# Kernel optimization log

Hardware: AMD Instinct MI355X
Metric: run time of the kernel (lower is better)

Reference implementation:

```python
import jax, jax.numpy as jnp
import numpy as np

B, S, D, H, V, L, N, FF = 4, 2048, 768, 4, 32000, 2048, 3, 1024
DH = D // H  # 192; note original scales scores by 1/20, not 1/sqrt(192)


def layernorm(x, g, b):
    m = jnp.mean(x, axis=-1, keepdims=True)
    v = jnp.mean((x - m) ** 2, axis=-1, keepdims=True)
    return (x - m) / jnp.sqrt(v + 1e-5) * g + b


def attn_block(h, Wq, bq, Wk, bk, Wv, bv, g, b, mask):
    Bx, Sx, _ = h.shape
    q = (h @ Wq + bq).reshape(Bx, Sx, H, DH).transpose(0, 2, 1, 3)  # bhsd
    k = (h @ Wk + bk).reshape(Bx, Sx, H, DH).transpose(0, 2, 1, 3)
    v = (h @ Wv + bv).reshape(Bx, Sx, H, DH).transpose(0, 2, 1, 3)
    w = jnp.einsum('bhqd,bhkd->bhqk', q, k) / 20.0
    w = jnp.where(mask, -1e9, w)
    # original code uses Softmax(dim=2), i.e. over the QUERY axis — kept faithful
    a = jax.nn.softmax(w, axis=2)
    o = jnp.einsum('bhqk,bhkd->bhqd', a, v)
    o = o.transpose(0, 2, 1, 3).reshape(Bx, Sx, D)
    return layernorm(h + o, g, b)


def setup_inputs() -> dict:
    key = jax.random.key(0)
    ks = jax.random.split(key, 12)
    sc = 0.02
    n = lambda k, s: jax.random.normal(k, s, jnp.float32) * sc
    return {
        'x': jax.random.randint(ks[0], (B, S), 0, V),
        'label': jax.random.randint(ks[1], (B, S), 0, V),
        'tok_emb': n(ks[2], (V, D)),
        'pos_emb': n(ks[3], (L, D)),
        'Wq': n(ks[4], (N, 2, D, D)), 'bq': jnp.zeros((N, 2, D)),
        'Wk': n(ks[5], (N, 2, D, D)), 'bk': jnp.zeros((N, 2, D)),
        'Wv': n(ks[6], (N, 2, D, D)), 'bv': jnp.zeros((N, 2, D)),
        'ln_g': jnp.ones((N, 2, D)), 'ln_b': jnp.zeros((N, 2, D)),
        'W1': n(ks[7], (N, D, FF)), 'b1': jnp.zeros((N, FF)),
        'W2': n(ks[8], (N, FF, D)), 'b2': jnp.zeros((N, D)),
        'f_g': jnp.ones((N, D)), 'f_b': jnp.zeros((N, D)),
        'Wcls': n(ks[9], (D, V)), 'bcls': jnp.zeros((V,)),
    }


def reference(x, label, tok_emb, pos_emb, Wq, bq, Wk, bk, Wv, bv, ln_g, ln_b,
              W1, b1, W2, b2, f_g, f_b, Wcls, bcls):
    Bx, Sx = x.shape
    pad = (x == 0)[:, None, :, None]                       # [B,1,S,1] masks query rows
    look = jnp.triu(jnp.ones((Sx, Sx), bool), 1)[None, None]
    mask = look | pad                                      # [B,1,S,S] -> broadcast over H
    h = tok_emb[x] + pos_emb[jnp.arange(Sx)][None, :, :]
    for i in range(N):
        for j in range(2):
            h = attn_block(h, Wq[i, j], bq[i, j], Wk[i, j], bk[i, j],
                           Wv[i, j], bv[i, j], ln_g[i, j], ln_b[i, j], mask)
        h1 = jax.nn.relu(h @ W1[i] + b1[i]) @ W2[i] + b2[i]
        h = layernorm(h + h1, f_g[i], f_b[i])
    logits = h @ Wcls + bcls                               # [B,S,V]
    logp = jax.nn.log_softmax(logits, axis=-1)
    loss = -jnp.mean(jnp.take_along_axis(logp, label[..., None], axis=-1))
    return loss
```

## Files before the change

### kernel.cpp

```cpp
#include <hip/hip_runtime.h>
#include <hip/hip_bf16.h>

using u16 = unsigned short;
using u32 = unsigned int;
using u8  = unsigned char;
using u64 = unsigned long long;
using bf16x8 = __attribute__((ext_vector_type(8))) short;
using f32x4  = __attribute__((ext_vector_type(4))) float;
using l2v    = __attribute__((ext_vector_type(2))) long;

namespace {
constexpr int BB   = 4;
constexpr int SEQ  = 2048;
constexpr int DIM  = 768;
constexpr int NH   = 4;
constexpr int DHD  = 192;
constexpr int VOC  = 32000;
constexpr int NLAY = 3;
constexpr int FFD  = 1024;
constexpr int ROWS = BB * SEQ;
constexpr int NT2  = VOC / 256;
constexpr int QKV = 3 * DIM;
constexpr int BH  = BB * NH;
}

__device__ __forceinline__ float b2f(u16 u) { return __uint_as_float(((u32)u) << 16); }
__device__ __forceinline__ u16 f2b(float f) {
    u32 x = __float_as_uint(f);
    return (u16)((x + 0x7fffu + ((x >> 16) & 1u)) >> 16);
}

__device__ __forceinline__ u32 f2e4m3(float f) {
    float af = fabsf(f);
    u32 sgn = (__float_as_uint(f) >> 24) & 0x80u;
    if (!(af < 448.f)) return sgn | 0x7Eu;
    int e = (int)((__float_as_uint(af) >> 23) & 0xff) - 127;
    if (e < -6) e = -6;
    float sc = __uint_as_float((u32)(130 - e) << 23);
    int code = __float2int_rn(af * sc) + ((e + 6) << 3);
    return sgn | (u32)code;
}

__device__ __forceinline__ void gload16(const u16* g, u16* l) {
    __builtin_amdgcn_global_load_lds(
        (const __attribute__((address_space(1))) u32*)g,
        (__attribute__((address_space(3))) u32*)l, 16, 0, 0);
}
__device__ __forceinline__ void gload16b(const u8* g, u8* l) {
    __builtin_amdgcn_global_load_lds(
        (const __attribute__((address_space(1))) u32*)g,
        (__attribute__((address_space(3))) u32*)l, 16, 0, 0);
}

#define PHASE_END(N) do {                                        \
    __builtin_amdgcn_sched_barrier(0);                           \
    asm volatile("s_waitcnt vmcnt(" #N ")" ::: "memory");        \
    __builtin_amdgcn_s_barrier();                                \
    asm volatile("" ::: "memory");                               \
    __builtin_amdgcn_sched_barrier(0);                           \
} while (0)

__device__ __forceinline__ float block_sum256(float v, float* sb) {
    #pragma unroll
    for (int off = 32; off > 0; off >>= 1) v += __shfl_down(v, off, 64);
    int lane = threadIdx.x & 63, w = threadIdx.x >> 6;
    if (lane == 0) sb[w] = v;
    __syncthreads();
    float r = sb[0] + sb[1] + sb[2] + sb[3];
    __syncthreads();
    return r;
}

template<int MODE>
__global__ __launch_bounds__(512, 2)
void gemm256(const u16* __restrict__ A, long lda,
             const u16* __restrict__ Bt, long ldb,
             int M, int N, int K,
             u16* __restrict__ Cb, long ldc,
             int HH, long sAb, long sAh, long sBb, long sBh, long sCb, long sCh,
             const int* __restrict__ xtok, float* __restrict__ cpart)
{
    __shared__ __align__(16) u16 sA[2][256 * 64];
    __shared__ __align__(16) u16 sB[2][256 * 64];

    int t = threadIdx.x, w = t >> 6, lane = t & 63;
    int wr = w >> 2, wcn = w & 3;
    int lr = lane & 15, lg = lane >> 4, rsw = lr & 7;

    int z = blockIdx.z;
    int bz = z / HH, hz = z % HH;
    const u16* Ab = A + (size_t)bz * sAb + (size_t)hz * sAh;
    const u16* Bb = Bt + (size_t)bz * sBb + (size_t)hz * sBh;
    size_t Coff = (size_t)bz * sCb + (size_t)hz * sCh;

    int bx = blockIdx.x, by = blockIdx.y;
    {
        int tix = blockIdx.x;
        by = 7;
        while (by * (by + 1) / 2 > tix) by--;
        bx = tix - by * (by + 1) / 2;
    }
    int m0 = by * 256, n0 = bx * 256;

    int srow = lane >> 3;
    int scol = ((lane & 7) ^ srow) * 8;

    f32x4 acc[8][4];
    #pragma unroll
    for (int i = 0; i < 8; i++)
        #pragma unroll
        for (int j = 0; j < 4; j++) acc[i][j] = (f32x4){0.f, 0.f, 0.f, 0.f};

    auto stageA = [&](int buf, int k0) {
        #pragma unroll
        for (int r = 0; r < 4; r++) {
            int rb = r * 64 + w * 8;
            gload16(Ab + (size_t)(m0 + rb + srow) * lda + k0 + scol,
                    &sA[buf][rb * 64]);
        }
    };
    auto stageB = [&](int buf, int k0, int h) {
        #pragma unroll
        for (int j = 0; j < 2; j++) {
            int rb = (j * 2 + (w >> 2)) * 64 + h * 32 + (w & 3) * 8;
            gload16(Bb + (size_t)(n0 + rb + srow) * ldb + k0 + scol,
                    &sB[buf][rb * 64]);
        }
    };

    {
        int nt = K >> 6;
        stageA(0, 0); stageB(0, 0, 0); stageB(0, 0, 1);
        PHASE_END(0);

        for (int kt = 0; kt < nt; ++kt) {
            int cur = kt & 1;
            int kn = (kt + 1) << 6;
            bool st = (kt + 1 < nt);
            bf16x8 aa[2][8], bb[2][2];
            #pragma unroll
            for (int kx = 0; kx < 2; kx++) {
                int jsw = ((kx * 4 + lg) ^ rsw) * 8;
                #pragma unroll
                for (int mi = 0; mi < 8; mi++)
                    aa[kx][mi] = *(const bf16x8*)&sA[cur][(wr * 128 + mi * 16 + lr) * 64 + jsw];
                #pragma unroll
                for (int ni = 0; ni < 2; ni++)
                    bb[kx][ni] = *(const bf16x8*)&sB[cur][(wcn * 64 + ni * 16 + lr) * 64 + jsw];
            }
            if (st) { stageA(cur ^ 1, kn); stageB(cur ^ 1, kn, 0); }
            __builtin_amdgcn_s_setprio(1);
            #pragma unroll
            for (int kx = 0; kx < 2; kx++)
                #pragma unroll
                for (int mi = 0; mi < 8; mi++)
                    #pragma unroll
                    for (int ni = 0; ni < 2; ni++)
                        acc[mi][ni] = __builtin_amdgcn_mfma_f32_16x16x32_bf16(
                            aa[kx][mi], bb[kx][ni], acc[mi][ni], 0, 0, 0);
            __builtin_amdgcn_s_setprio(0);
            if (st) PHASE_END(6); else PHASE_END(0);

            bf16x8 bc[2][2];
            #pragma unroll
            for (int kx = 0; kx < 2; kx++) {
                int jsw = ((kx * 4 + lg) ^ rsw) * 8;
                #pragma unroll
                for (int ni = 0; ni < 2; ni++)
                    bc[kx][ni] = *(const bf16x8*)&sB[cur][(wcn * 64 + (ni + 2) * 16 + lr) * 64 + jsw];
            }
            if (st) stageB(cur ^ 1, kn, 1);
            __builtin_amdgcn_s_setprio(1);
            #pragma unroll
            for (int kx = 0; kx < 2; kx++)
                #pragma unroll
                for (int mi = 0; mi < 8; mi++)
                    #pragma unroll
                    for (int ni = 0; ni < 2; ni++)
                        acc[mi][ni + 2] = __builtin_amdgcn_mfma_f32_16x16x32_bf16(
                            aa[kx][mi], bc[kx][ni], acc[mi][ni + 2], 0, 0, 0);
            __builtin_amdgcn_s_setprio(0);
            if (st) PHASE_END(2); else PHASE_END(0);
        }
    }

    {
        const int* xb = xtok + (size_t)bz * SEQ;
        float cs[2][4] = {{0.f,0.f,0.f,0.f},{0.f,0.f,0.f,0.f}};
        #pragma unroll
        for (int mi = 0; mi < 8; mi++)
            #pragma unroll
            for (int j = 0; j < 4; j++) {
                int grow = m0 + wr * 128 + mi * 16 + lg * 4 + j;
                int xz = xb[grow];
                #pragma unroll
                for (int ni = 0; ni < 4; ni++) {
                    int gcol = n0 + wcn * 64 + ni * 16 + lr;
                    float v = acc[mi][ni][j] * 0.05f;
                    if (gcol > grow || xz == 0) v = -30.f;
                    float e = __expf(v);
                    Cb[Coff + (size_t)grow * ldc + gcol] = f2b(e);
                    cs[mi >> 2][ni] += e;
                }
            }
        #pragma unroll
        for (int h = 0; h < 2; h++)
            #pragma unroll
            for (int ni = 0; ni < 4; ni++) {
                float c = cs[h][ni];
                c += __shfl_xor(c, 16, 64);
                c += __shfl_xor(c, 32, 64);
                if (lg == 0) {
                    int p = (m0 >> 6) + wr * 2 + h;
                    cpart[((size_t)p * BH + z) * SEQ + n0 + wcn * 64 + ni * 16 + lr] = c;
                }
            }
    }
}

__global__ __launch_bounds__(512, 2)
void gemm256_f8(const u8* __restrict__ Aq, const u8* __restrict__ Bq, int K,
                const float* __restrict__ bias,
                const int* __restrict__ label,
                float* __restrict__ partials, float* __restrict__ picked)
{
    __shared__ __align__(16) u8 sA8[2][256 * 128];
    __shared__ __align__(16) u8 sB8[2][2][128 * 128];

    int t = threadIdx.x, w = t >> 6, lane = t & 63;
    int wr = w >> 2, wcn = w & 3;
    int lr = lane & 15, lg = lane >> 4;
    int rx = lr & 7;

    int bx = blockIdx.x, by = blockIdx.y;
    {
        int pid = by * gridDim.x + bx;
        int xcd = pid & 7, s = pid >> 3;
        bx = s >> 2;
        by = xcd * 4 + (s & 3);
    }
    int m0 = by * 256, n0 = bx * 256;

    int srow8 = lane >> 3;
    int scol8 = ((lane & 7) ^ srow8) * 16;

    f32x4 acc[8][4];
    #pragma unroll
    for (int i = 0; i < 8; i++)
        #pragma unroll
        for (int j = 0; j < 4; j++) acc[i][j] = (f32x4){0.f, 0.f, 0.f, 0.f};

    auto stageA = [&](int buf, int k0) {
        #pragma unroll
        for (int i = 0; i < 4; i++) {
            int rb = i * 64 + w * 8;
            gload16b(Aq + (size_t)(m0 + rb + srow8) * DIM + k0 + scol8,
                     &sA8[buf][rb * 128]);
        }
    };
    auto stageB = [&](int buf, int k0, int h) {
        #pragma unroll
        for (int j = 0; j < 2; j++) {
            int rh = j * 64 + w * 8;
            int rbase = (rh >> 5) * 64 + h * 32 + (rh & 31);
            gload16b(Bq + (size_t)(n0 + rbase + srow8) * DIM + k0 + scol8,
                     &sB8[buf][h][rh * 128]);
        }
    };

    int nt = K >> 7;
    stageA(0, 0); stageB(0, 0, 0); stageB(0, 0, 1);
    PHASE_END(0);

    for (int kt = 0; kt < nt; ++kt) {
        int cur = kt & 1;
        int kn = (kt + 1) << 7;
        bool st = (kt + 1 < nt);
        l2v aa[2][8], bb[2][2];
        #pragma unroll
        for (int h = 0; h < 2; h++) {
            int off = ((2 * lg + h) ^ rx) * 16;
            #pragma unroll
            for (int mi = 0; mi < 8; mi++)
                aa[h][mi] = *(const l2v*)&sA8[cur][(wr * 128 + mi * 16 + lr) * 128 + off];
            #pragma unroll
            for (int ni = 0; ni < 2; ni++)
                bb[h][ni] = *(const l2v*)&sB8[cur][0][(wcn * 32 + ni * 16 + lr) * 128 + off];
        }
        if (st) { stageA(cur ^ 1, kn); stageB(cur ^ 1, kn, 0); }
        __builtin_amdgcn_s_setprio(1);
        #pragma unroll
        for (int h = 0; h < 2; h++)
            #pragma unroll
            for (int e = 0; e < 2; e++)
                #pragma unroll
                for (int mi = 0; mi < 8; mi++)
                    #pragma unroll
                    for (int ni = 0; ni < 2; ni++)
                        acc[mi][ni] = __builtin_amdgcn_mfma_f32_16x16x32_fp8_fp8(
                            aa[h][mi][e], bb[h][ni][e], acc[mi][ni], 0, 0, 0);
        __builtin_amdgcn_s_setprio(0);
        if (st) PHASE_END(6); else PHASE_END(0);
        l2v bc[2][2];
        #pragma unroll
        for (int h = 0; h < 2; h++) {
            int off = ((2 * lg + h) ^ rx) * 16;
            #pragma unroll
            for (int ni = 0; ni < 2; ni++)
                bc[h][ni] = *(const l2v*)&sB8[cur][1][(wcn * 32 + ni * 16 + lr) * 128 + off];
        }
        if (st) stageB(cur ^ 1, kn, 1);
        __builtin_amdgcn_s_setprio(1);
        #pragma unroll
        for (int h = 0; h < 2; h++)
            #pragma unroll
            for (int e = 0; e < 2; e++)
                #pragma unroll
                for (int mi = 0; mi < 8; mi++)
                    #pragma unroll
                    for (int ni = 0; ni < 2; ni++)
                        acc[mi][ni + 2] = __builtin_amdgcn_mfma_f32_16x16x32_fp8_fp8(
                            aa[h][mi][e], bc[h][ni][e], acc[mi][ni + 2], 0, 0, 0);
        __builtin_amdgcn_s_setprio(0);
        if (st) PHASE_END(2); else PHASE_END(0);
    }

    #pragma unroll
    for (int mi = 0; mi < 8; mi++)
        #pragma unroll
        for (int ni = 0; ni < 4; ni++) {
            int gcol = n0 + wcn * 64 + ni * 16 + lr;
            float bcol = bias[gcol];
            #pragma unroll
            for (int j = 0; j < 4; j++)
                acc[mi][ni][j] = acc[mi][ni][j] * (1.f / 64.f) + bcol;
        }
    #pragma unroll
    for (int mi = 0; mi < 8; mi++)
        #pragma unroll
        for (int j = 0; j < 4; j++) {
            int grow = m0 + wr * 128 + mi * 16 + lg * 4 + j;
            int lab = label[grow];
            #pragma unroll
            for (int ni = 0; ni < 4; ni++) {
                int gcol = n0 + wcn * 64 + ni * 16 + lr;
                if (lab == gcol) picked[grow] = acc[mi][ni][j];
            }
        }
    float* red = (float*)sA8;
    #pragma unroll
    for (int mi = 0; mi < 8; mi++)
        #pragma unroll
        for (int j = 0; j < 4; j++) {
            float mx = -1e30f;
            #pragma unroll
            for (int ni = 0; ni < 4; ni++) mx = fmaxf(mx, acc[mi][ni][j]);
            #pragma unroll
            for (int off = 1; off < 16; off <<= 1)
                mx = fmaxf(mx, __shfl_xor(mx, off, 64));
            float ss = 0.f;
            #pragma unroll
            for (int ni = 0; ni < 4; ni++) ss += __expf(acc[mi][ni][j] - mx);
            #pragma unroll
            for (int off = 1; off < 16; off <<= 1) ss += __shfl_xor(ss, off, 64);
            if (lr == 0) {
                int rloc = wr * 128 + mi * 16 + lg * 4 + j;
                red[rloc * 8 + wcn * 2 + 0] = mx;
                red[rloc * 8 + wcn * 2 + 1] = ss;
            }
        }
    __syncthreads();
    if (t < 256) {
        float Mv = -1e30f;
        #pragma unroll
        for (int q = 0; q < 4; q++) Mv = fmaxf(Mv, red[t * 8 + q * 2]);
        float Sv = 0.f;
        #pragma unroll
        for (int q = 0; q < 4; q++)
            Sv += red[t * 8 + q * 2 + 1] * __expf(red[t * 8 + q * 2] - Mv);
        size_t row = (size_t)(m0 + t);
        partials[(row * NT2 + bx) * 2 + 0] = Mv;
        partials[(row * NT2 + bx) * 2 + 1] = Sv;
    }
}

template<int MODE>
__global__ __launch_bounds__(256)
void gemm128(const u16* __restrict__ A, long lda,
             const u16* __restrict__ Bt, long ldb,
             int N, int K,
             const float* __restrict__ bias,
             u16* __restrict__ Cb, long ldc, int relu,
             int HH, long sAb, long sAh, long sBb, long sBh, long sCb, long sCh)
{
    __shared__ __align__(16) u16 sA[2][128 * 64];
    __shared__ __align__(16) u16 sB[2][128 * 64];

    int z = blockIdx.z, bz = z / HH, hz = z % HH;
    const u16* Ab = A + (size_t)bz * sAb + (size_t)hz * sAh;
    const u16* Bb = Bt + (size_t)bz * sBb + (size_t)hz * sBh;
    size_t Coff = (size_t)bz * sCb + (size_t)hz * sCh;

    int bx = blockIdx.x, by = blockIdx.y;
    if (MODE == 0 && gridDim.y == 64) {
        int pid = by * gridDim.x + bx;
        int xcd = pid & 7, s = pid >> 3;
        bx = s >> 3;
        by = xcd * 8 + (s & 7);
    }
    if (MODE == 3) {
        by = (by & 1) ? (15 - (by >> 1)) : (by >> 1);
    }
    int m0 = by * 128, n0 = bx * 128;

    int t = threadIdx.x, w = t >> 6, lane = t & 63;
    int wr = w >> 1, wc = w & 1, lr = lane & 15, lg = lane >> 4, rsw = lr & 7;
    int srow = lane >> 3, scol = ((lane & 7) ^ srow) * 8;

    f32x4 acc[4][4];
    #pragma unroll
    for (int i = 0; i < 4; i++)
        #pragma unroll
        for (int j = 0; j < 4; j++) acc[i][j] = (f32x4){0.f, 0.f, 0.f, 0.f};

    auto stageA = [&](int buf, int k0) {
        #pragma unroll
        for (int i = 0; i < 4; i++) {
            int rb = (w * 4 + i) * 8;
            gload16(Ab + (size_t)(m0 + rb + srow) * lda + k0 + scol,
                    &sA[buf][rb * 64]);
        }
    };
    auto stageB = [&](int buf, int k0, int h) {
        #pragma unroll
        for (int j = 0; j < 2; j++) {
            int rb = j * 64 + h * 32 + w * 8;
            int row = n0 + rb + srow;
            if (MODE == 3) { if (row > N - 1) row = N - 1; }
            gload16(Bb + (size_t)row * ldb + k0 + scol, &sB[buf][rb * 64]);
        }
    };

    int nt = K >> 6;
    if (MODE == 3) {
        int ntE = (by + 1) * 2;
        if (ntE < nt) nt = ntE;
    }

    stageA(0, 0); stageB(0, 0, 0); stageB(0, 0, 1);
    PHASE_END(0);

    for (int kt = 0; kt < nt; ++kt) {
        int cur = kt & 1;
        int kn = (kt + 1) << 6;
        bool st = (kt + 1 < nt);
        bf16x8 aa[2][4], bb[2][2];
        #pragma unroll
        for (int kx = 0; kx < 2; kx++) {
            int jsw = ((kx * 4 + lg) ^ rsw) * 8;
            #pragma unroll
            for (int mi = 0; mi < 4; mi++)
                aa[kx][mi] = *(const bf16x8*)&sA[cur][(wr * 64 + mi * 16 + lr) * 64 + jsw];
            #pragma unroll
            for (int ni = 0; ni < 2; ni++)
                bb[kx][ni] = *(const bf16x8*)&sB[cur][(wc * 64 + ni * 16 + lr) * 64 + jsw];
        }
        if (st) { stageA(cur ^ 1, kn); stageB(cur ^ 1, kn, 0); }
        __builtin_amdgcn_s_setprio(1);
        #pragma unroll
        for (int kx = 0; kx < 2; kx++)
            #pragma unroll
            for (int mi = 0; mi < 4; mi++)
                #pragma unroll
                for (int ni = 0; ni < 2; ni++)
                    acc[mi][ni] = __builtin_amdgcn_mfma_f32_16x16x32_bf16(
                        aa[kx][mi], bb[kx][ni], acc[mi][ni], 0, 0, 0);
        __builtin_amdgcn_s_setprio(0);
        if (st) PHASE_END(6); else PHASE_END(0);

        bf16x8 bc[2][2];
        #pragma unroll
        for (int kx = 0; kx < 2; kx++) {
            int jsw = ((kx * 4 + lg) ^ rsw) * 8;
            #pragma unroll
            for (int ni = 0; ni < 2; ni++)
                bc[kx][ni] = *(const bf16x8*)&sB[cur][(wc * 64 + (ni + 2) * 16 + lr) * 64 + jsw];
        }
        if (st) stageB(cur ^ 1, kn, 1);
        __builtin_amdgcn_s_setprio(1);
        #pragma unroll
        for (int kx = 0; kx < 2; kx++)
            #pragma unroll
            for (int mi = 0; mi < 4; mi++)
                #pragma unroll
                for (int ni = 0; ni < 2; ni++)
                    acc[mi][ni + 2] = __builtin_amdgcn_mfma_f32_16x16x32_bf16(
                        aa[kx][mi], bc[kx][ni], acc[mi][ni + 2], 0, 0, 0);
        __builtin_amdgcn_s_setprio(0);
        if (st) PHASE_END(2); else PHASE_END(0);
    }

    #pragma unroll
    for (int mi = 0; mi < 4; mi++)
        #pragma unroll
        for (int ni = 0; ni < 4; ni++)
            #pragma unroll
            for (int j = 0; j < 4; j++) {
                int grow = m0 + wr * 64 + mi * 16 + lg * 4 + j;
                int gcol = n0 + wc * 64 + ni * 16 + lr;
                if (MODE == 3) {
                    if (gcol < N)
                        Cb[Coff + (size_t)grow * ldc + gcol] = f2b(acc[mi][ni][j]);
                } else {
                    float v = acc[mi][ni][j];
                    if (bias) v += bias[gcol];
                    if (relu) v = fmaxf(v, 0.f);
                    Cb[Coff + (size_t)grow * ldc + gcol] = f2b(v);
                }
            }
}

__global__ __launch_bounds__(256)
void embed_k(const int* __restrict__ x, const float* __restrict__ tok,
             const float* __restrict__ pos, u16* __restrict__ hb)
{
    int row = blockIdx.x, t = threadIdx.x;
    int token = x[row];
    int s = row & (SEQ - 1);
    size_t base = (size_t)row * DIM;
    #pragma unroll
    for (int e = 0; e < 3; e++) {
        int d = t + e * 256;
        float v = tok[(size_t)token * DIM + d] + pos[(size_t)s * DIM + d];
        hb[base + d] = f2b(v);
    }
}

__global__ __launch_bounds__(256)
void resid_ln(const u16* __restrict__ res, const u16* __restrict__ add,
              const float* __restrict__ g, const float* __restrict__ b,
              u16* __restrict__ out)
{
    __shared__ float sb[4];
    int row = blockIdx.x, t = threadIdx.x;
    size_t base = (size_t)row * DIM;
    float x0 = 0.f, x1 = 0.f, x2 = 0.f, x3 = 0.f;
    if (t < 192) {
        ushort4 r4 = *(const ushort4*)&res[base + t * 4];
        ushort4 a4 = *(const ushort4*)&add[base + t * 4];
        x0 = b2f(r4.x) + b2f(a4.x);
        x1 = b2f(r4.y) + b2f(a4.y);
        x2 = b2f(r4.z) + b2f(a4.z);
        x3 = b2f(r4.w) + b2f(a4.w);
    }
    float mean = block_sum256(x0 + x1 + x2 + x3, sb) * (1.f / DIM);
    float d0 = x0 - mean, d1 = x1 - mean, d2 = x2 - mean, d3 = x3 - mean;
    float var = block_sum256(t < 192 ? d0*d0 + d1*d1 + d2*d2 + d3*d3 : 0.f, sb) * (1.f / DIM);
    float rs = rsqrtf(var + 1e-5f);
    if (t < 192) {
        float4 gv = *(const float4*)&g[t * 4];
        float4 bv = *(const float4*)&b[t * 4];
        ushort4 ob = {f2b(d0 * rs * gv.x + bv.x), f2b(d1 * rs * gv.y + bv.y),
                      f2b(d2 * rs * gv.z + bv.z), f2b(d3 * rs * gv.w + bv.w)};
        *(ushort4*)&out[base + t * 4] = ob;
    }
}

__global__ __launch_bounds__(256)
void h_to_fp8(const u16* __restrict__ hb, u8* __restrict__ hq)
{
    size_t idx = (size_t)blockIdx.x * 256 + threadIdx.x;
    bf16x8 v = *(const bf16x8*)&hb[idx * 8];
    u64 o = 0;
    #pragma unroll
    for (int e = 0; e < 8; e++)
        o |= (u64)f2e4m3(b2f((u16)v[e]) * 4.f) << (8 * e);
    *(u64*)&hq[idx * 8] = o;
}

__global__ void v_transpose(const u16* __restrict__ v, long ldv,
                            const float* __restrict__ cpart, u16* __restrict__ vT)
{
    __shared__ u16 tile[32][33];
    int z = blockIdx.z;
    int b = z >> 2, h = z & 3;
    int s0 = blockIdx.x * 32, d0 = blockIdx.y * 32;
    int tx = threadIdx.x, ty = threadIdx.y;
    #pragma unroll
    for (int i = 0; i < 4; i++)
        tile[ty + i * 8][tx] = v[((size_t)b * SEQ + s0 + ty + i * 8) * ldv + h * DHD + d0 + tx];
    int scol = s0 + tx;
    int pmin = (scol >> 8) * 4;
    float sv = 0.f;
    for (int p = pmin; p < 32; p++) sv += cpart[((size_t)p * BH + z) * SEQ + scol];
    float inv = 1.f / sv;
    __syncthreads();
    #pragma unroll
    for (int i = 0; i < 4; i++)
        vT[((size_t)z * DHD + d0 + ty + i * 8) * SEQ + scol] =
            f2b(b2f(tile[tx][ty + i * 8]) * inv);
}

__global__ void wt_cvt(const float* __restrict__ src, u16* __restrict__ dst, int K, int N)
{
    __shared__ float tile[32][33];
    int n0 = blockIdx.x * 32, k0 = blockIdx.y * 32;
    int tx = threadIdx.x, ty = threadIdx.y;
    #pragma unroll
    for (int i = 0; i < 4; i++)
        tile[ty + i * 8][tx] = src[(size_t)(k0 + ty + i * 8) * N + n0 + tx];
    __syncthreads();
    #pragma unroll
    for (int i = 0; i < 4; i++)
        dst[(size_t)(n0 + ty + i * 8) * K + k0 + tx] = f2b(tile[tx][ty + i * 8]);
}

__global__ void wt_cvt8(const float* __restrict__ src, u8* __restrict__ dst, int K, int N)
{
    __shared__ float tile[32][33];
    int n0 = blockIdx.x * 32, k0 = blockIdx.y * 32;
    int tx = threadIdx.x, ty = threadIdx.y;
    #pragma unroll
    for (int i = 0; i < 4; i++)
        tile[ty + i * 8][tx] = src[(size_t)(k0 + ty + i * 8) * N + n0 + tx];
    __syncthreads();
    #pragma unroll
    for (int i = 0; i < 4; i++)
        dst[(size_t)(n0 + ty + i * 8) * K + k0 + tx] =
            (u8)f2e4m3(tile[tx][ty + i * 8] * 16.f);
}

__global__ __launch_bounds__(256)
void bias_cat(const float* __restrict__ bq, const float* __restrict__ bk,
              const float* __restrict__ bv, float* __restrict__ dst)
{
    int ij = blockIdx.x, t = threadIdx.x;
    #pragma unroll
    for (int e = 0; e < 3; e++) {
        int d = t + e * 256;
        dst[(size_t)ij * QKV + d]            = bq[(size_t)ij * DIM + d];
        dst[(size_t)ij * QKV + DIM + d]      = bk[(size_t)ij * DIM + d];
        dst[(size_t)ij * QKV + 2 * DIM + d]  = bv[(size_t)ij * DIM + d];
    }
}

__global__ __launch_bounds__(256)
void lse_merge(const float* __restrict__ partials, float* __restrict__ lse)
{
    __shared__ float sm[4], ssum[4];
    int row = blockIdx.x, t = threadIdx.x;
    float m = -1e30f, s = 0.f;
    if (t < NT2) {
        const float* p = partials + ((size_t)row * NT2 + t) * 2;
        m = p[0]; s = p[1];
    }
    #pragma unroll
    for (int off = 1; off < 64; off <<= 1) {
        float om = __shfl_xor(m, off, 64), os = __shfl_xor(s, off, 64);
        float M = fmaxf(m, om);
        s = s * __expf(m - M) + os * __expf(om - M);
        m = M;
    }
    int lane = t & 63, w = t >> 6;
    if (lane == 0) { sm[w] = m; ssum[w] = s; }
    __syncthreads();
    if (t == 0) {
        float M = fmaxf(fmaxf(sm[0], sm[1]), fmaxf(sm[2], sm[3]));
        float S = ssum[0] * __expf(sm[0] - M) + ssum[1] * __expf(sm[1] - M) +
                  ssum[2] * __expf(sm[2] - M) + ssum[3] * __expf(sm[3] - M);
        lse[row] = M + __logf(S);
    }
}

__global__ __launch_bounds__(256)
void loss_k(const float* __restrict__ lse, const float* __restrict__ picked,
            float* __restrict__ out)
{
    __shared__ float sb[4];
    int t = threadIdx.x;
    float a = 0.f;
    for (int r = t; r < ROWS; r += 256) a += lse[r] - picked[r];
    float tot = block_sum256(a, sb);
    if (t == 0) out[0] = tot / (float)ROWS;
}

extern "C" void kernel_launch(void* const* d_in, const int* in_sizes, int n_in,
                              void* d_out, int out_size, void* d_ws, size_t ws_size,
                              hipStream_t stream)
{
    (void)in_sizes; (void)n_in; (void)out_size; (void)ws_size;
    const int*   x     = (const int*)d_in[0];
    const int*   label = (const int*)d_in[1];
    const float* tok   = (const float*)d_in[2];
    const float* pos   = (const float*)d_in[3];
    const float* Wq    = (const float*)d_in[4];
    const float* bq    = (const float*)d_in[5];
    const float* Wk    = (const float*)d_in[6];
    const float* bk    = (const float*)d_in[7];
    const float* Wv    = (const float*)d_in[8];
    const float* bv    = (const float*)d_in[9];
    const float* ln_g  = (const float*)d_in[10];
    const float* ln_b  = (const float*)d_in[11];
    const float* W1    = (const float*)d_in[12];
    const float* b1    = (const float*)d_in[13];
    const float* W2    = (const float*)d_in[14];
    const float* b2    = (const float*)d_in[15];
    const float* f_g   = (const float*)d_in[16];
    const float* f_b   = (const float*)d_in[17];
    const float* Wcls  = (const float*)d_in[18];
    const float* bcls  = (const float*)d_in[19];

    char* p = (char*)d_ws;
    auto alloc = [&](size_t bytes) -> char* {
        char* r = p;
        p += (bytes + 255) & ~(size_t)255;
        return r;
    };
    u16* hb     = (u16*)alloc((size_t)ROWS * DIM * 2);
    u16* ob     = (u16*)alloc((size_t)ROWS * DIM * 2);
    u16* qkvb   = (u16*)alloc((size_t)ROWS * QKV * 2);
    u16* vTb    = (u16*)alloc((size_t)BH * DHD * SEQ * 2);
    u16* ff1b   = (u16*)alloc((size_t)ROWS * FFD * 2);
    u16* wbuf   = (u16*)alloc((size_t)BH * SEQ * SEQ * 2);
    u16* WqkvT  = (u16*)alloc((size_t)6 * QKV * DIM * 2);
    u16* W1T    = (u16*)alloc((size_t)NLAY * DIM * FFD * 2);
    u16* W2T    = (u16*)alloc((size_t)NLAY * FFD * DIM * 2);
    u8*  WcT8   = (u8*)alloc((size_t)DIM * VOC);
    u8*  hq     = (u8*)alloc((size_t)ROWS * DIM);
    float* bqkv = (float*)alloc((size_t)6 * QKV * 4);
    float* cpart= (float*)alloc((size_t)32 * BH * SEQ * 4);
    float* partials = (float*)alloc((size_t)ROWS * NT2 * 2 * 4);
    float* picked   = (float*)alloc((size_t)ROWS * 4);
    float* lsev     = (float*)alloc((size_t)ROWS * 4);

    dim3 t32(32, 8, 1);
    for (int ij = 0; ij < 6; ij++) {
        wt_cvt<<<dim3(DIM / 32, DIM / 32, 1), t32, 0, stream>>>(
            Wq + (size_t)ij * DIM * DIM, WqkvT + (size_t)ij * QKV * DIM, DIM, DIM);
        wt_cvt<<<dim3(DIM / 32, DIM / 32, 1), t32, 0, stream>>>(
            Wk + (size_t)ij * DIM * DIM, WqkvT + (size_t)ij * QKV * DIM + (size_t)DIM * DIM, DIM, DIM);
        wt_cvt<<<dim3(DIM / 32, DIM / 32, 1), t32, 0, stream>>>(
            Wv + (size_t)ij * DIM * DIM, WqkvT + (size_t)ij * QKV * DIM + (size_t)2 * DIM * DIM, DIM, DIM);
    }
    bias_cat<<<6, 256, 0, stream>>>(bq, bk, bv, bqkv);
    for (int i = 0; i < NLAY; i++) {
        wt_cvt<<<dim3(FFD / 32, DIM / 32, 1), t32, 0, stream>>>(
            W1 + (size_t)i * DIM * FFD, W1T + (size_t)i * DIM * FFD, DIM, FFD);
        wt_cvt<<<dim3(DIM / 32, FFD / 32, 1), t32, 0, stream>>>(
            W2 + (size_t)i * FFD * DIM, W2T + (size_t)i * FFD * DIM, FFD, DIM);
    }
    wt_cvt8<<<dim3(VOC / 32, DIM / 32, 1), t32, 0, stream>>>(Wcls, WcT8, DIM, VOC);

    embed_k<<<ROWS, 256, 0, stream>>>(x, tok, pos, hb);

    for (int i = 0; i < NLAY; i++) {
        for (int j = 0; j < 2; j++) {
            int ij = i * 2 + j;
            gemm128<0><<<dim3(QKV / 128, ROWS / 128, 1), 256, 0, stream>>>(
                hb, DIM, WqkvT + (size_t)ij * QKV * DIM, DIM, QKV, DIM,
                bqkv + (size_t)ij * QKV, qkvb, QKV, 0,
                1, 0, 0, 0, 0, 0, 0);
            gemm256<1><<<dim3(36, 1, BH), 512, 0, stream>>>(
                qkvb, QKV, qkvb + DIM, QKV, SEQ, SEQ, DHD,
                wbuf, SEQ,
                NH, (long)SEQ * QKV, (long)DHD, (long)SEQ * QKV, (long)DHD,
                (long)NH * SEQ * SEQ, (long)SEQ * SEQ,
                x, cpart);
            v_transpose<<<dim3(SEQ / 32, DHD / 32, BH), t32, 0, stream>>>(
                qkvb + 2 * DIM, QKV, cpart, vTb);
            gemm128<3><<<dim3(2, SEQ / 128, BH), 256, 0, stream>>>(
                wbuf, SEQ, vTb, SEQ, DHD, SEQ,
                nullptr, ob, DIM, 0,
                NH, (long)NH * SEQ * SEQ, (long)SEQ * SEQ,
                (long)NH * DHD * SEQ, (long)DHD * SEQ,
                (long)SEQ * DIM, (long)DHD);
            resid_ln<<<ROWS, 256, 0, stream>>>(
                hb, ob, ln_g + (size_t)ij * DIM, ln_b + (size_t)ij * DIM, hb);
        }
        gemm128<0><<<dim3(FFD / 128, ROWS / 128, 1), 256, 0, stream>>>(
            hb, DIM, W1T + (size_t)i * DIM * FFD, DIM, FFD, DIM,
            b1 + (size_t)i * FFD, ff1b, FFD, 1,
            1, 0, 0, 0, 0, 0, 0);
        gemm128<0><<<dim3(DIM / 128, ROWS / 128, 1), 256, 0, stream>>>(
            ff1b, FFD, W2T + (size_t)i * FFD * DIM, FFD, DIM, FFD,
            b2 + (size_t)i * DIM, ob, DIM, 0,
            1, 0, 0, 0, 0, 0, 0);
        resid_ln<<<ROWS, 256, 0, stream>>>(
            hb, ob, f_g + (size_t)i * DIM, f_b + (size_t)i * DIM, hb);
    }

    h_to_fp8<<<(ROWS * DIM / 8) / 256, 256, 0, stream>>>(hb, hq);
    gemm256_f8<<<dim3(NT2, ROWS / 256, 1), 512, 0, stream>>>(
        hq, WcT8, DIM, bcls, label, partials, picked);
    lse_merge<<<ROWS, 256, 0, stream>>>(partials, lsev);
    loss_k<<<1, 256, 0, stream>>>(lsev, picked, (float*)d_out);
}
```

Baseline: 2.030 ms.

## Split fp8 classifier GEMM k-step into four quarter-tile phases with interleaved staging

```diff
diff --git a/kernel.cpp b/kernel.cpp
--- a/kernel.cpp
+++ b/kernel.cpp
@@ -60,6 +60,13 @@
     __builtin_amdgcn_sched_barrier(0);                           \
 } while (0)
 
+#define GBAR() do {                                              \
+    __builtin_amdgcn_sched_barrier(0);                           \
+    __builtin_amdgcn_s_barrier();                                \
+    asm volatile("" ::: "memory");                               \
+    __builtin_amdgcn_sched_barrier(0);                           \
+} while (0)
+
 __device__ __forceinline__ float block_sum256(float v, float* sb) {
     #pragma unroll
     for (int off = 32; off > 0; off >>= 1) v += __shfl_down(v, off, 64);
@@ -250,15 +257,15 @@
         #pragma unroll
         for (int j = 0; j < 4; j++) acc[i][j] = (f32x4){0.f, 0.f, 0.f, 0.f};
 
-    auto stageA = [&](int buf, int k0) {
-        #pragma unroll
-        for (int i = 0; i < 4; i++) {
-            int rb = i * 64 + w * 8;
+    auto stageA2 = [&](int buf, int k0, int par) {
+        #pragma unroll
+        for (int i = 0; i < 2; i++) {
+            int rb = (par + i * 2) * 64 + w * 8;
             gload16b(Aq + (size_t)(m0 + rb + srow8) * DIM + k0 + scol8,
                      &sA8[buf][rb * 128]);
         }
     };
-    auto stageB = [&](int buf, int k0, int h) {
+    auto stageBh = [&](int buf, int k0, int h) {
         #pragma unroll
         for (int j = 0; j < 2; j++) {
             int rh = j * 64 + w * 8;
@@ -267,62 +274,69 @@
                      &sB8[buf][h][rh * 128]);
         }
     };
-
-    int nt = K >> 7;
-    stageA(0, 0); stageB(0, 0, 0); stageB(0, 0, 1);
-    PHASE_END(0);
-
-    for (int kt = 0; kt < nt; ++kt) {
-        int cur = kt & 1;
-        int kn = (kt + 1) << 7;
-        bool st = (kt + 1 < nt);
-        l2v aa[2][8], bb[2][2];
+    auto rdA = [&](int cur, int mh, l2v (&aa)[2][4]) {
         #pragma unroll
         for (int h = 0; h < 2; h++) {
             int off = ((2 * lg + h) ^ rx) * 16;
             #pragma unroll
-            for (int mi = 0; mi < 8; mi++)
-                aa[h][mi] = *(const l2v*)&sA8[cur][(wr * 128 + mi * 16 + lr) * 128 + off];
-            #pragma unroll
-            for (int ni = 0; ni < 2; ni++)
-                bb[h][ni] = *(const l2v*)&sB8[cur][0][(wcn * 32 + ni * 16 + lr) * 128 + off];
-        }
-        if (st) { stageA(cur ^ 1, kn); stageB(cur ^ 1, kn, 0); }
+            for (int i = 0; i < 4; i++)
+                aa[h][i] = *(const l2v*)&sA8[cur][(wr * 128 + (mh * 4 + i) * 16 + lr) * 128 + off];
+        }
+    };
+    auto rdB = [&](int cur, int nh, l2v (&bb)[2][2]) {
+        #pragma unroll
+        for (int h = 0; h < 2; h++) {
+            int off = ((2 * lg + h) ^ rx) * 16;
+            #pragma unroll
+            for (int i = 0; i < 2; i++)
+                bb[h][i] = *(const l2v*)&sB8[cur][nh][(wcn * 32 + i * 16 + lr) * 128 + off];
+        }
+    };
+    auto mfma32 = [&](const l2v (&aa)[2][4], const l2v (&bb)[2][2], int mh, int nh) {
         __builtin_amdgcn_s_setprio(1);
         #pragma unroll
         for (int h = 0; h < 2; h++)
             #pragma unroll
             for (int e = 0; e < 2; e++)
                 #pragma unroll
-                for (int mi = 0; mi < 8; mi++)
+                for (int i = 0; i < 4; i++)
                     #pragma unroll
-                    for (int ni = 0; ni < 2; ni++)
-                        acc[mi][ni] = __builtin_amdgcn_mfma_f32_16x16x32_fp8_fp8(
-                            aa[h][mi][e], bb[h][ni][e], acc[mi][ni], 0, 0, 0);
+                    for (int j = 0; j < 2; j++)
+                        acc[mh * 4 + i][nh * 2 + j] =
+                            __builtin_amdgcn_mfma_f32_16x16x32_fp8_fp8(
+                                aa[h][i][e], bb[h][j][e],
+                                acc[mh * 4 + i][nh * 2 + j], 0, 0, 0);
         __builtin_amdgcn_s_setprio(0);
-        if (st) PHASE_END(6); else PHASE_END(0);
-        l2v bc[2][2];
-        #pragma unroll
-        for (int h = 0; h < 2; h++) {
-            int off = ((2 * lg + h) ^ rx) * 16;
-            #pragma unroll
-            for (int ni = 0; ni < 2; ni++)
-                bc[h][ni] = *(const l2v*)&sB8[cur][1][(wcn * 32 + ni * 16 + lr) * 128 + off];
-        }
-        if (st) stageB(cur ^ 1, kn, 1);
-        __builtin_amdgcn_s_setprio(1);
-        #pragma unroll
-        for (int h = 0; h < 2; h++)
-            #pragma unroll
-            for (int e = 0; e < 2; e++)
-                #pragma unroll
-                for (int mi = 0; mi < 8; mi++)
-                    #pragma unroll
-                    for (int ni = 0; ni < 2; ni++)
-                        acc[mi][ni + 2] = __builtin_amdgcn_mfma_f32_16x16x32_fp8_fp8(
-                            aa[h][mi][e], bc[h][ni][e], acc[mi][ni + 2], 0, 0, 0);
-        __builtin_amdgcn_s_setprio(0);
-        if (st) PHASE_END(2); else PHASE_END(0);
+    };
+
+    int nt = K >> 7;
+    stageA2(0, 0, 0); stageBh(0, 0, 0); stageA2(0, 0, 1); stageBh(0, 0, 1);
+    PHASE_END(4);
+
+    for (int kt = 0; kt < nt; ++kt) {
+        int cur = kt & 1, kn = (kt + 1) << 7;
+        bool st = kt + 1 < nt;
+        l2v aa[2][4], bb[2][2];
+        rdA(cur, 0, aa); rdB(cur, 0, bb);
+        if (st) stageA2(cur ^ 1, kn, 0);
+        GBAR();
+        mfma32(aa, bb, 0, 0);
+        if (st) PHASE_END(4); else PHASE_END(2);
+        rdA(cur, 1, aa);
+        if (st) stageBh(cur ^ 1, kn, 0);
+        GBAR();
+        mfma32(aa, bb, 1, 0);
+        if (st) PHASE_END(4); else PHASE_END(0);
+        rdA(cur, 0, aa); rdB(cur, 1, bb);
+        if (st) stageA2(cur ^ 1, kn, 1);
+        GBAR();
+        mfma32(aa, bb, 0, 1);
+        PHASE_END(6);
+        rdA(cur, 1, aa);
+        if (st) stageBh(cur ^ 1, kn, 1);
+        GBAR();
+        mfma32(aa, bb, 1, 1);
+        if (st) PHASE_END(4); else PHASE_END(0);
     }
 
     #pragma unroll
```

After: 2.099 ms. +3.4%, slower.

## Run QKV and FFN projections in FP8 with quantization fused into producers

Applied to the files above, without the earlier changes.

```diff
diff --git a/kernel.cpp b/kernel.cpp
--- a/kernel.cpp
+++ b/kernel.cpp
@@ -384,6 +384,129 @@
     }
 }
 
+__global__ __launch_bounds__(256)
+void gemm128_f8(const u8* __restrict__ Aq, const u8* __restrict__ Bq,
+                int K,
+                const float* __restrict__ bias,
+                u16* __restrict__ Cb, u8* __restrict__ Cq, long ldc, int relu)
+{
+    __shared__ __align__(16) u8 sA8[2][128 * 128];
+    __shared__ __align__(16) u8 sB8[2][2][64 * 128];
+
+    int t = threadIdx.x, w = t >> 6, lane = t & 63;
+    int wr = w >> 1, wc = w & 1;
+    int lr = lane & 15, lg = lane >> 4;
+    int rx = lr & 7;
+
+    int bx = blockIdx.x, by = blockIdx.y;
+    {
+        int pid = by * gridDim.x + bx;
+        int xcd = pid & 7, s = pid >> 3;
+        bx = s >> 3;
+        by = xcd * 8 + (s & 7);
+    }
+    int m0 = by * 128, n0 = bx * 128;
+
+    int srow8 = lane >> 3;
+    int scol8 = ((lane & 7) ^ srow8) * 16;
+
+    f32x4 acc[4][4];
+    #pragma unroll
+    for (int i = 0; i < 4; i++)
+        #pragma unroll
+        for (int j = 0; j < 4; j++) acc[i][j] = (f32x4){0.f, 0.f, 0.f, 0.f};
+
+    auto stageA = [&](int buf, int k0) {
+        #pragma unroll
+        for (int i = 0; i < 4; i++) {
+            int rb = i * 32 + w * 8;
+            gload16b(Aq + (size_t)(m0 + rb + srow8) * K + k0 + scol8,
+                     &sA8[buf][rb * 128]);
+        }
+    };
+    auto stageB = [&](int buf, int k0, int h) {
+        #pragma unroll
+        for (int j = 0; j < 2; j++) {
+            int rh = j * 32 + w * 8;
+            int rbase = j * 64 + h * 32 + w * 8;
+            gload16b(Bq + (size_t)(n0 + rbase + srow8) * K + k0 + scol8,
+                     &sB8[buf][h][rh * 128]);
+        }
+    };
+
+    int nt = K >> 7;
+    stageA(0, 0); stageB(0, 0, 0); stageB(0, 0, 1);
+    PHASE_END(0);
+
+    for (int kt = 0; kt < nt; ++kt) {
+        int cur = kt & 1;
+        int kn = (kt + 1) << 7;
+        bool st = (kt + 1 < nt);
+        l2v aa[2][4], bb[2][2];
+        #pragma unroll
+        for (int h = 0; h < 2; h++) {
+            int off = ((2 * lg + h) ^ rx) * 16;
+            #pragma unroll
+            for (int mi = 0; mi < 4; mi++)
+                aa[h][mi] = *(const l2v*)&sA8[cur][(wr * 64 + mi * 16 + lr) * 128 + off];
+            #pragma unroll
+            for (int ni = 0; ni < 2; ni++)
+                bb[h][ni] = *(const l2v*)&sB8[cur][0][(wc * 32 + ni * 16 + lr) * 128 + off];
+        }
+        if (st) { stageA(cur ^ 1, kn); stageB(cur ^ 1, kn, 0); }
+        __builtin_amdgcn_s_setprio(1);
+        #pragma unroll
+        for (int h = 0; h < 2; h++)
+            #pragma unroll
+            for (int e = 0; e < 2; e++)
+                #pragma unroll
+                for (int mi = 0; mi < 4; mi++)
+                    #pragma unroll
+                    for (int ni = 0; ni < 2; ni++)
+                        acc[mi][ni] = __builtin_amdgcn_mfma_f32_16x16x32_fp8_fp8(
+                            aa[h][mi][e], bb[h][ni][e], acc[mi][ni], 0, 0, 0);
+        __builtin_amdgcn_s_setprio(0);
+        if (st) PHASE_END(6); else PHASE_END(0);
+        l2v bc[2][2];
+        #pragma unroll
+        for (int h = 0; h < 2; h++) {
+            int off = ((2 * lg + h) ^ rx) * 16;
+            #pragma unroll
+            for (int ni = 0; ni < 2; ni++)
+                bc[h][ni] = *(const l2v*)&sB8[cur][1][(wc * 32 + ni * 16 + lr) * 128 + off];
+        }
+        if (st) stageB(cur ^ 1, kn, 1);
+        __builtin_amdgcn_s_setprio(1);
+        #pragma unroll
+        for (int h = 0; h < 2; h++)
+            #pragma unroll
+            for (int e = 0; e < 2; e++)
+                #pragma unroll
+                for (int mi = 0; mi < 4; mi++)
+                    #pragma unroll
+                    for (int ni = 0; ni < 2; ni++)
+                        acc[mi][ni + 2] = __builtin_amdgcn_mfma_f32_16x16x32_fp8_fp8(
+                            aa[h][mi][e], bc[h][ni][e], acc[mi][ni + 2], 0, 0, 0);
+        __builtin_amdgcn_s_setprio(0);
+        if (st) PHASE_END(2); else PHASE_END(0);
+    }
+
+    #pragma unroll
+    for (int mi = 0; mi < 4; mi++)
+        #pragma unroll
+        for (int ni = 0; ni < 4; ni++)
+            #pragma unroll
+            for (int j = 0; j < 4; j++) {
+                int grow = m0 + wr * 64 + mi * 16 + lg * 4 + j;
+                int gcol = n0 + wc * 64 + ni * 16 + lr;
+                float v = acc[mi][ni][j] * (1.f / 64.f) + bias[gcol];
+                if (relu) v = fmaxf(v, 0.f);
+                size_t ci = (size_t)grow * ldc + gcol;
+                if (Cb) Cb[ci] = f2b(v);
+                if (Cq) Cq[ci] = (u8)f2e4m3(v * 4.f);
+            }
+}
+
 template<int MODE>
 __global__ __launch_bounds__(256)
 void gemm128(const u16* __restrict__ A, long lda,
@@ -402,12 +525,6 @@
     size_t Coff = (size_t)bz * sCb + (size_t)hz * sCh;
 
     int bx = blockIdx.x, by = blockIdx.y;
-    if (MODE == 0 && gridDim.y == 64) {
-        int pid = by * gridDim.x + bx;
-        int xcd = pid & 7, s = pid >> 3;
-        bx = s >> 3;
-        by = xcd * 8 + (s & 7);
-    }
     if (MODE == 3) {
         by = (by & 1) ? (15 - (by >> 1)) : (by >> 1);
     }
@@ -508,21 +625,14 @@
             for (int j = 0; j < 4; j++) {
                 int grow = m0 + wr * 64 + mi * 16 + lg * 4 + j;
                 int gcol = n0 + wc * 64 + ni * 16 + lr;
-                if (MODE == 3) {
-                    if (gcol < N)
-                        Cb[Coff + (size_t)grow * ldc + gcol] = f2b(acc[mi][ni][j]);
-                } else {
-                    float v = acc[mi][ni][j];
-                    if (bias) v += bias[gcol];
-                    if (relu) v = fmaxf(v, 0.f);
-                    Cb[Coff + (size_t)grow * ldc + gcol] = f2b(v);
-                }
+                if (gcol < N)
+                    Cb[Coff + (size_t)grow * ldc + gcol] = f2b(acc[mi][ni][j]);
             }
 }
 
 __global__ __launch_bounds__(256)
 void embed_k(const int* __restrict__ x, const float* __restrict__ tok,
-             const float* __restrict__ pos, u16* __restrict__ hb)
+             const float* __restrict__ pos, u16* __restrict__ hb, u8* __restrict__ hq)
 {
     int row = blockIdx.x, t = threadIdx.x;
     int token = x[row];
@@ -533,13 +643,14 @@
         int d = t + e * 256;
         float v = tok[(size_t)token * DIM + d] + pos[(size_t)s * DIM + d];
         hb[base + d] = f2b(v);
+        hq[base + d] = (u8)f2e4m3(v * 4.f);
     }
 }
 
 __global__ __launch_bounds__(256)
 void resid_ln(const u16* __restrict__ res, const u16* __restrict__ add,
               const float* __restrict__ g, const float* __restrict__ b,
-              u16* __restrict__ out)
+              u16* __restrict__ out, u8* __restrict__ outq)
 {
     __shared__ float sb[4];
     int row = blockIdx.x, t = threadIdx.x;
@@ -560,22 +671,14 @@
     if (t < 192) {
         float4 gv = *(const float4*)&g[t * 4];
         float4 bv = *(const float4*)&b[t * 4];
-        ushort4 ob = {f2b(d0 * rs * gv.x + bv.x), f2b(d1 * rs * gv.y + bv.y),
-                      f2b(d2 * rs * gv.z + bv.z), f2b(d3 * rs * gv.w + bv.w)};
+        float y0 = d0 * rs * gv.x + bv.x, y1 = d1 * rs * gv.y + bv.y;
+        float y2 = d2 * rs * gv.z + bv.z, y3 = d3 * rs * gv.w + bv.w;
+        ushort4 ob = {f2b(y0), f2b(y1), f2b(y2), f2b(y3)};
         *(ushort4*)&out[base + t * 4] = ob;
-    }
-}
-
-__global__ __launch_bounds__(256)
-void h_to_fp8(const u16* __restrict__ hb, u8* __restrict__ hq)
-{
-    size_t idx = (size_t)blockIdx.x * 256 + threadIdx.x;
-    bf16x8 v = *(const bf16x8*)&hb[idx * 8];
-    u64 o = 0;
-    #pragma unroll
-    for (int e = 0; e < 8; e++)
-        o |= (u64)f2e4m3(b2f((u16)v[e]) * 4.f) << (8 * e);
-    *(u64*)&hq[idx * 8] = o;
+        uchar4 oq = {(u8)f2e4m3(y0 * 4.f), (u8)f2e4m3(y1 * 4.f),
+                     (u8)f2e4m3(y2 * 4.f), (u8)f2e4m3(y3 * 4.f)};
+        *(uchar4*)&outq[base + t * 4] = oq;
+    }
 }
 
 __global__ void v_transpose(const u16* __restrict__ v, long ldv,
@@ -601,23 +704,12 @@
             f2b(b2f(tile[tx][ty + i * 8]) * inv);
 }
 
-__global__ void wt_cvt(const float* __restrict__ src, u16* __restrict__ dst, int K, int N)
+__global__ void wt_cvt8_z(const float* __restrict__ src0, long sSrc,
+                          u8* __restrict__ dst0, long sDst, int K, int N)
 {
     __shared__ float tile[32][33];
-    int n0 = blockIdx.x * 32, k0 = blockIdx.y * 32;
-    int tx = threadIdx.x, ty = threadIdx.y;
-    #pragma unroll
-    for (int i = 0; i < 4; i++)
-        tile[ty + i * 8][tx] = src[(size_t)(k0 + ty + i * 8) * N + n0 + tx];
-    __syncthreads();
-    #pragma unroll
-    for (int i = 0; i < 4; i++)
-        dst[(size_t)(n0 + ty + i * 8) * K + k0 + tx] = f2b(tile[tx][ty + i * 8]);
-}
-
-__global__ void wt_cvt8(const float* __restrict__ src, u8* __restrict__ dst, int K, int N)
-{
-    __shared__ float tile[32][33];
+    const float* src = src0 + (size_t)blockIdx.z * sSrc;
+    u8* dst = dst0 + (size_t)blockIdx.z * sDst;
     int n0 = blockIdx.x * 32, k0 = blockIdx.y * 32;
     int tx = threadIdx.x, ty = threadIdx.y;
     #pragma unroll
@@ -717,16 +809,16 @@
         return r;
     };
     u16* hb     = (u16*)alloc((size_t)ROWS * DIM * 2);
+    u8*  hq     = (u8*)alloc((size_t)ROWS * DIM);
     u16* ob     = (u16*)alloc((size_t)ROWS * DIM * 2);
     u16* qkvb   = (u16*)alloc((size_t)ROWS * QKV * 2);
     u16* vTb    = (u16*)alloc((size_t)BH * DHD * SEQ * 2);
-    u16* ff1b   = (u16*)alloc((size_t)ROWS * FFD * 2);
+    u8*  ff1q   = (u8*)alloc((size_t)ROWS * FFD);
     u16* wbuf   = (u16*)alloc((size_t)BH * SEQ * SEQ * 2);
-    u16* WqkvT  = (u16*)alloc((size_t)6 * QKV * DIM * 2);
-    u16* W1T    = (u16*)alloc((size_t)NLAY * DIM * FFD * 2);
-    u16* W2T    = (u16*)alloc((size_t)NLAY * FFD * DIM * 2);
+    u8*  WqkvT8 = (u8*)alloc((size_t)6 * QKV * DIM);
+    u8*  W1T8   = (u8*)alloc((size_t)NLAY * DIM * FFD);
+    u8*  W2T8   = (u8*)alloc((size_t)NLAY * FFD * DIM);
     u8*  WcT8   = (u8*)alloc((size_t)DIM * VOC);
-    u8*  hq     = (u8*)alloc((size_t)ROWS * DIM);
     float* bqkv = (float*)alloc((size_t)6 * QKV * 4);
     float* cpart= (float*)alloc((size_t)32 * BH * SEQ * 4);
     float* partials = (float*)alloc((size_t)ROWS * NT2 * 2 * 4);
@@ -734,32 +826,28 @@
     float* lsev     = (float*)alloc((size_t)ROWS * 4);
 
     dim3 t32(32, 8, 1);
-    for (int ij = 0; ij < 6; ij++) {
-        wt_cvt<<<dim3(DIM / 32, DIM / 32, 1), t32, 0, stream>>>(
-            Wq + (size_t)ij * DIM * DIM, WqkvT + (size_t)ij * QKV * DIM, DIM, DIM);
-        wt_cvt<<<dim3(DIM / 32, DIM / 32, 1), t32, 0, stream>>>(
-            Wk + (size_t)ij * DIM * DIM, WqkvT + (size_t)ij * QKV * DIM + (size_t)DIM * DIM, DIM, DIM);
-        wt_cvt<<<dim3(DIM / 32, DIM / 32, 1), t32, 0, stream>>>(
-            Wv + (size_t)ij * DIM * DIM, WqkvT + (size_t)ij * QKV * DIM + (size_t)2 * DIM * DIM, DIM, DIM);
-    }
+    wt_cvt8_z<<<dim3(DIM / 32, DIM / 32, 6), t32, 0, stream>>>(
+        Wq, (long)DIM * DIM, WqkvT8, (long)QKV * DIM, DIM, DIM);
+    wt_cvt8_z<<<dim3(DIM / 32, DIM / 32, 6), t32, 0, stream>>>(
+        Wk, (long)DIM * DIM, WqkvT8 + (size_t)DIM * DIM, (long)QKV * DIM, DIM, DIM);
+    wt_cvt8_z<<<dim3(DIM / 32, DIM / 32, 6), t32, 0, stream>>>(
+        Wv, (long)DIM * DIM, WqkvT8 + (size_t)2 * DIM * DIM, (long)QKV * DIM, DIM, DIM);
+    wt_cvt8_z<<<dim3(FFD / 32, DIM / 32, NLAY), t32, 0, stream>>>(
+        W1, (long)DIM * FFD, W1T8, (long)DIM * FFD, DIM, FFD);
+    wt_cvt8_z<<<dim3(DIM / 32, FFD / 32, NLAY), t32, 0, stream>>>(
+        W2, (long)FFD * DIM, W2T8, (long)FFD * DIM, FFD, DIM);
+    wt_cvt8_z<<<dim3(VOC / 32, DIM / 32, 1), t32, 0, stream>>>(
+        Wcls, 0L, WcT8, 0L, DIM, VOC);
     bias_cat<<<6, 256, 0, stream>>>(bq, bk, bv, bqkv);
-    for (int i = 0; i < NLAY; i++) {
-        wt_cvt<<<dim3(FFD / 32, DIM / 32, 1), t32, 0, stream>>>(
-            W1 + (size_t)i * DIM * FFD, W1T + (size_t)i * DIM * FFD, DIM, FFD);
-        wt_cvt<<<dim3(DIM / 32, FFD / 32, 1), t32, 0, stream>>>(
-            W2 + (size_t)i * FFD * DIM, W2T + (size_t)i * FFD * DIM, FFD, DIM);
-    }
-    wt_cvt8<<<dim3(VOC / 32, DIM / 32, 1), t32, 0, stream>>>(Wcls, WcT8, DIM, VOC);
-
-    embed_k<<<ROWS, 256, 0, stream>>>(x, tok, pos, hb);
+
+    embed_k<<<ROWS, 256, 0, stream>>>(x, tok, pos, hb, hq);
 
     for (int i = 0; i < NLAY; i++) {
         for (int j = 0; j < 2; j++) {
             int ij = i * 2 + j;
-            gemm128<0><<<dim3(QKV / 128, ROWS / 128, 1), 256, 0, stream>>>(
-                hb, DIM, WqkvT + (size_t)ij * QKV * DIM, DIM, QKV, DIM,
-                bqkv + (size_t)ij * QKV, qkvb, QKV, 0,
-                1, 0, 0, 0, 0, 0, 0);
+            gemm128_f8<<<dim3(QKV / 128, ROWS / 128, 1), 256, 0, stream>>>(
+                hq, WqkvT8 + (size_t)ij * QKV * DIM, DIM,
+                bqkv + (size_t)ij * QKV, qkvb, nullptr, QKV, 0);
             gemm256<1><<<dim3(36, 1, BH), 512, 0, stream>>>(
                 qkvb, QKV, qkvb + DIM, QKV, SEQ, SEQ, DHD,
                 wbuf, SEQ,
@@ -775,21 +863,18 @@
                 (long)NH * DHD * SEQ, (long)DHD * SEQ,
                 (long)SEQ * DIM, (long)DHD);
             resid_ln<<<ROWS, 256, 0, stream>>>(
-                hb, ob, ln_g + (size_t)ij * DIM, ln_b + (size_t)ij * DIM, hb);
-        }
-        gemm128<0><<<dim3(FFD / 128, ROWS / 128, 1), 256, 0, stream>>>(
-            hb, DIM, W1T + (size_t)i * DIM * FFD, DIM, FFD, DIM,
-            b1 + (size_t)i * FFD, ff1b, FFD, 1,
-            1, 0, 0, 0, 0, 0, 0);
-        gemm128<0><<<dim3(DIM / 128, ROWS / 128, 1), 256, 0, stream>>>(
-            ff1b, FFD, W2T + (size_t)i * FFD * DIM, FFD, DIM, FFD,
-            b2 + (size_t)i * DIM, ob, DIM, 0,
-            1, 0, 0, 0, 0, 0, 0);
+                hb, ob, ln_g + (size_t)ij * DIM, ln_b + (size_t)ij * DIM, hb, hq);
+        }
+        gemm128_f8<<<dim3(FFD / 128, ROWS / 128, 1), 256, 0, stream>>>(
+            hq, W1T8 + (size_t)i * DIM * FFD, DIM,
+            b1 + (size_t)i * FFD, nullptr, ff1q, FFD, 1);
+        gemm128_f8<<<dim3(DIM / 128, ROWS / 128, 1), 256, 0, stream>>>(
+            ff1q, W2T8 + (size_t)i * FFD * DIM, FFD,
+            b2 + (size_t)i * DIM, ob, nullptr, DIM, 0);
         resid_ln<<<ROWS, 256, 0, stream>>>(
-            hb, ob, f_g + (size_t)i * DIM, f_b + (size_t)i * DIM, hb);
-    }
-
-    h_to_fp8<<<(ROWS * DIM / 8) / 256, 256, 0, stream>>>(hb, hq);
+            hb, ob, f_g + (size_t)i * DIM, f_b + (size_t)i * DIM, hb, hq);
+    }
+
     gemm256_f8<<<dim3(NT2, ROWS / 256, 1), 512, 0, stream>>>(
         hq, WcT8, DIM, bcls, label, partials, picked);
     lse_merge<<<ROWS, 256, 0, stream>>>(partials, lsev);
```

After: 1.727 ms. -14.9%, faster.
